# Kernel tuning notes

Measured on AMD Instinct MI355X. Metric: run time of the kernel, lower is better.

## Reference

```python
import jax, jax.numpy as jnp
import numpy as np

N = 131072       # total nodes (B graphs x P nodes)
P = 4096         # nodes per graph
B = 32           # graphs in batch
E = 2097152      # edges (avg degree 16)
IN_DIM = 64
HID = 128
OUT = 16
EPS = 1e-5
SLOPE = 0.01


def _degrees(idx):
    # structural degree, clamped to min 1 (as DGL GraphConv does)
    d = jax.ops.segment_sum(jnp.ones((E,), jnp.float32), idx, num_segments=N)
    return jnp.maximum(d, 1.0)


def _graph_conv(x, W, src, dst, ew):
    # DGL GraphConv, norm='both', bias=False, with scalar edge weights:
    # h = D_out^{-1/2} x ; m_v = sum_{(u->v)} w_e h_u ; out = (D_in^{-1/2} m) W
    h = x * jax.lax.rsqrt(_degrees(src))[:, None]
    m = jax.ops.segment_sum(ew[:, None] * h[src], dst, num_segments=N)  # [N, F]
    return (m * jax.lax.rsqrt(_degrees(dst))[:, None]) @ W


def _graph_norm(x, gamma, beta, alpha):
    # GraphNorm (Cai et al. / PyG, batch=None): stats over all nodes per feature
    mu = jnp.mean(x, axis=0)
    c = x - alpha * mu
    var = jnp.mean(c * c, axis=0)
    return c * jax.lax.rsqrt(var + EPS) * gamma + beta


def _mean_nodes(h, gid):
    # per-graph mean readout; every graph has exactly P nodes
    return jax.ops.segment_sum(h, gid, num_segments=B) / P


def setup_inputs() -> dict:
    key = jax.random.key(0)
    ks = jax.random.split(key, 8)
    src = jax.random.randint(ks[0], (E,), 0, N, dtype=jnp.int32)
    # keep edges within each 4096-node graph block (batched DGL graph)
    dst = (src // P) * P + jax.random.randint(ks[1], (E,), 0, P, dtype=jnp.int32)
    features = jax.random.normal(ks[2], (N, IN_DIM), jnp.float32)
    edge_weights = jax.random.uniform(ks[3], (E,), jnp.float32)
    # kaiming/xavier-scale init approximations
    W1 = jax.random.normal(ks[4], (IN_DIM, HID), jnp.float32) * np.sqrt(2.0 / IN_DIM)
    W2 = jax.random.normal(ks[5], (HID, HID), jnp.float32) * np.sqrt(2.0 / HID)
    Wc = jax.random.normal(ks[6], (OUT, 2 * HID), jnp.float32) * np.sqrt(1.0 / (2 * HID))
    ones = jnp.ones((HID,), jnp.float32)
    zeros = jnp.zeros((HID,), jnp.float32)
    return {
        'features': features, 'edge_weights': edge_weights, 'src': src, 'dst': dst,
        'W1': W1, 'W2': W2, 'Wc': Wc,
        'gamma1': ones, 'beta1': zeros, 'alpha1': ones,
        'gamma2': ones, 'beta2': zeros, 'alpha2': ones,
    }


def reference(features, edge_weights, src, dst, W1, W2, Wc,
              gamma1, beta1, alpha1, gamma2, beta2, alpha2):
    gid = jnp.arange(N, dtype=jnp.int32) // P  # node -> graph id
    h1 = _graph_conv(features, W1, src, dst, edge_weights)
    h1 = jax.nn.leaky_relu(_graph_norm(h1, gamma1, beta1, alpha1), SLOPE)
    r1 = _mean_nodes(h1, gid)                  # [B, HID]
    h2 = _graph_conv(h1, W2, src, dst, edge_weights)
    h2 = jax.nn.leaky_relu(_graph_norm(h2, gamma2, beta2, alpha2), SLOPE)
    r2 = _mean_nodes(h2, gid)                  # [B, HID]
    readouts = jnp.concatenate([r1, r2], axis=1)  # [B, 2*HID]
    return readouts @ Wc.T                     # [B, OUT]
```

## Files before the change

### kernel.cpp

```cpp
#include <hip/hip_runtime.h>
#include <hip/hip_fp16.h>

constexpr int NN   = 131072;
constexpr int PP   = 4096;
constexpr int BG   = 32;
constexpr int EE   = 2097152;
constexpr int IND  = 64;
constexpr int HH   = 128;
constexpr int CAP  = 81920;
constexpr float EPSV   = 1e-5f;
constexpr float SLOPEV = 0.01f;

typedef short bf16x8 __attribute__((ext_vector_type(8)));
typedef float f32x4  __attribute__((ext_vector_type(4)));
typedef float f32x2  __attribute__((ext_vector_type(2)));

__device__ __forceinline__ unsigned f2bf(float f) {
    unsigned u = __float_as_uint(f);
    return (u + 0x7FFFu + ((u >> 16) & 1u)) >> 16;
}
__device__ __forceinline__ unsigned pack2bf(float lo, float hi) {
    return f2bf(lo) | (f2bf(hi) << 16);
}
__device__ __forceinline__ float bflo(unsigned p) { return __uint_as_float(p << 16); }
__device__ __forceinline__ float bfhi(unsigned p) { return __uint_as_float(p & 0xFFFF0000u); }
__device__ __forceinline__ float w16(unsigned r) {
    return __half2float(__ushort_as_half((unsigned short)(r >> 16)));
}

template <int K>
__device__ __forceinline__ void packw_body(const float* __restrict__ W,
                                           unsigned short* __restrict__ pw, int t) {
    if (t >= K * 16) return;
    int lane = t & 63, nt = (t >> 6) & 7, kt = t >> 9;
    int kbase = kt * 32 + ((lane >> 4) & 3) * 8;
    int col   = nt * 16 + (lane & 15);
    for (int j = 0; j < 8; j++)
        pw[t * 8 + j] = (unsigned short)f2bf(W[(kbase + j) * HH + col]);
}

__global__ __launch_bounds__(256) void k_prep(const float* __restrict__ features,
                                              unsigned* __restrict__ f8x,
                                              const float* __restrict__ W1,
                                              unsigned short* __restrict__ pw1,
                                              const float* __restrict__ W2,
                                              unsigned short* __restrict__ pw2,
                                              int* __restrict__ gcur,
                                              float* __restrict__ racc,
                                              unsigned* __restrict__ csr2) {
    int b = blockIdx.x, t = threadIdx.x;
    if (b < 8192) {
        int i = b * 256 + t;
        float4 v = ((const float4*)features)[i];
        int w0 = __builtin_amdgcn_cvt_pk_fp8_f32(v.x, v.y, 0, false);
        int w1 = __builtin_amdgcn_cvt_pk_fp8_f32(v.z, v.w, w0, true);
        f8x[i] = (unsigned)w1;
        return;
    }
    if (b == 8192) {
        if (t < BG) gcur[t * 16] = t * CAP;
        for (int i = t; i < 2 * BG * HH; i += 256) racc[i] = 0.f;
        return;
    }
    if (b < 8197) { packw_body<64>(W1, pw1, (b - 8193) * 256 + t); return; }
    if (b < 8205) { packw_body<128>(W2, pw2, (b - 8197) * 256 + t); return; }
    ((uint4*)csr2)[(b - 8205) * 256 + t] = make_uint4(0, 0, 0, 0);
}

__global__ __launch_bounds__(256) void k_part(const int* __restrict__ src,
                                              const int* __restrict__ dst,
                                              const float* __restrict__ ew,
                                              int* __restrict__ gcur,
                                              uint2* __restrict__ recs) {
    __shared__ int cnt[32];
    __shared__ int start[32];
    __shared__ int gbase[32];
    __shared__ uint2 stage[4096];
    int t = threadIdx.x;
    int ebase = blockIdx.x * 4096;
    if (t < 32) cnt[t] = 0;
    __syncthreads();
    int es[16]; int ed[16]; float ev[16];
#pragma unroll
    for (int k = 0; k < 16; k++) {
        int e = ebase + k * 256 + t;
        es[k] = src[e]; ed[k] = dst[e]; ev[k] = ew[e];
        atomicAdd(&cnt[es[k] >> 12], 1);
    }
    __syncthreads();
    if (t == 0) {
        int run = 0;
        for (int g = 0; g < 32; g++) { start[g] = run; run += cnt[g]; }
    }
    __syncthreads();
    if (t < 32) {
        gbase[t] = atomicAdd(&gcur[t * 16], cnt[t]);
        cnt[t] = start[t];
    }
    __syncthreads();
#pragma unroll
    for (int k = 0; k < 16; k++) {
        int g = es[k] >> 12;
        int pos = atomicAdd(&cnt[g], 1);
        stage[pos] = make_uint2((unsigned)(es[k] & 4095) | ((unsigned)(ed[k] & 4095) << 12) |
                                ((unsigned)g << 24), __float_as_uint(ev[k]));
    }
    __syncthreads();
    for (int i = t; i < 4096; i += 256) {
        uint2 r = stage[i];
        int g = r.x >> 24;
        recs[gbase[g] + (i - start[g])] = r;
    }
}

__global__ __launch_bounds__(1024) void k_hist(const uint2* __restrict__ recs,
                                               const int* __restrict__ gcur,
                                               int* __restrict__ shist,
                                               int* __restrict__ dhist) {
    __shared__ int hs[4096];
    __shared__ int hd[4096];
    int t = threadIdx.x;
    int g = blockIdx.x >> 3, c = blockIdx.x & 7;
    int n = gcur[g * 16] - g * CAP;
    int lo = (n * c) >> 3, hi = (n * (c + 1)) >> 3;
    ((int4*)hs)[t] = make_int4(0, 0, 0, 0);
    ((int4*)hd)[t] = make_int4(0, 0, 0, 0);
    __syncthreads();
    const uint2* base = recs + (size_t)g * CAP;
    for (int i = lo + t; i < hi; i += 1024) {
        unsigned x = base[i].x;
        atomicAdd(&hs[x & 4095], 1);
        atomicAdd(&hd[(x >> 12) & 4095], 1);
    }
    __syncthreads();
    ((int4*)(shist + (size_t)blockIdx.x * 4096))[t] = ((int4*)hs)[t];
    ((int4*)(dhist + (size_t)blockIdx.x * 4096))[t] = ((int4*)hd)[t];
}

__global__ __launch_bounds__(1024) void k_offs(int* __restrict__ shist,
                                               int* __restrict__ dhist,
                                               float* __restrict__ rs_s,
                                               float* __restrict__ rsd,
                                               int* __restrict__ degd,
                                               int* __restrict__ offs) {
    __shared__ int partial[1024];
    int t = threadIdx.x, g = blockIdx.x;
    int sdeg[4] = {0, 0, 0, 0}, ddeg[4] = {0, 0, 0, 0};
#pragma unroll
    for (int c = 0; c < 8; c++) {
        int4 sv = ((const int4*)(shist + (size_t)(g * 8 + c) * 4096))[t];
        int4 dv = ((const int4*)(dhist + (size_t)(g * 8 + c) * 4096))[t];
        sdeg[0] += sv.x; sdeg[1] += sv.y; sdeg[2] += sv.z; sdeg[3] += sv.w;
        ddeg[0] += dv.x; ddeg[1] += dv.y; ddeg[2] += dv.z; ddeg[3] += dv.w;
    }
    int pdeg[4];
#pragma unroll
    for (int j = 0; j < 4; j++) {
        int idx = t * 4 + j;
        int vs = sdeg[j]; if (vs < 1) vs = 1;
        rs_s[g * PP + idx] = rsqrtf((float)vs);
        int vd = ddeg[j]; if (vd < 1) vd = 1;
        rsd[g * PP + idx]  = rsqrtf((float)vd);
        pdeg[j] = (ddeg[j] + 3) & ~3;
        degd[g * PP + idx] = pdeg[j];
    }
    partial[t] = pdeg[0] + pdeg[1] + pdeg[2] + pdeg[3];
    __syncthreads();
    for (int off = 1; off < 1024; off <<= 1) {
        int v = partial[t];
        int add = (t >= off) ? partial[t - off] : 0;
        __syncthreads();
        partial[t] = v + add;
        __syncthreads();
    }
    int run = (t == 0) ? 0 : partial[t - 1];
#pragma unroll
    for (int j = 0; j < 4; j++) {
        int idx = t * 4 + j;
        offs[g * PP + idx] = g * CAP + run;
        int nb = run;
        for (int c = 0; c < 8; c++) {
            size_t hidx = (size_t)(g * 8 + c) * 4096 + idx;
            int v = dhist[hidx];
            dhist[hidx] = nb;
            nb += v;
        }
        run += pdeg[j];
    }
}

__global__ __launch_bounds__(1024) void k_place(const uint2* __restrict__ recs,
                                                const int* __restrict__ gcur,
                                                const int* __restrict__ dhist,
                                                const float* __restrict__ rs_s,
                                                unsigned* __restrict__ csr2) {
    __shared__ int cur[4096];
    __shared__ float rss[4096];
    int t = threadIdx.x;
    int g = blockIdx.x >> 3, c = blockIdx.x & 7;
    int n = gcur[g * 16] - g * CAP;
    int lo = (n * c) >> 3, hi = (n * (c + 1)) >> 3;
    ((int4*)cur)[t] = ((const int4*)(dhist + (size_t)blockIdx.x * 4096))[t];
    ((float4*)rss)[t] = ((const float4*)(rs_s + (size_t)g * PP))[t];
    __syncthreads();
    const uint2* base = recs + (size_t)g * CAP;
    unsigned* cbase = csr2 + (size_t)g * CAP;
    for (int i = lo + t; i < hi; i += 1024) {
        uint2 r = base[i];
        int sl = r.x & 4095, dl = (r.x >> 12) & 4095;
        int pos = atomicAdd(&cur[dl], 1);
        float wf = __uint_as_float(r.y) * rss[sl];
        cbase[pos] = (unsigned)sl | ((unsigned)__half_as_ushort(__float2half(wf)) << 16);
    }
}

__global__ __launch_bounds__(256) void k_aggemm1(const unsigned* __restrict__ f8x,
                                                 const unsigned* __restrict__ csr2,
                                                 const int* __restrict__ offs,
                                                 const int* __restrict__ degd,
                                                 const float* __restrict__ rsd,
                                                 const short* __restrict__ PW,
                                                 unsigned short* __restrict__ C,
                                                 float* __restrict__ part) {
    constexpr int WP = 36;
    __shared__ unsigned lds[64 * WP];
    __shared__ float s1[HH], s2[HH];
    int t = threadIdx.x;
    if (t < HH) { s1[t] = 0.f; s2[t] = 0.f; }
    int bid = blockIdx.x;
    int xcd = bid & 7, idx = bid >> 3;
    int g = xcd * 4 + (idx >> 6);
    int node0 = g * PP + (idx & 63) * 64;
    int lane = t & 63, wv = t >> 6;
    int q = lane >> 4, ql = lane & 15;
    const unsigned* hp8 = f8x + (size_t)((unsigned)(g * PP)) * 16 + ql;
    for (int p = 0; p < 2; p++) {
        int lrA = wv * 16 + p * 8 + q * 2;
        int va = node0 + lrA, vb = va + 1;
        int oa = offs[va], ca = degd[va];
        int ob = offs[vb], cb = degd[vb];
        float A0 = 0.f, A1 = 0.f, A2 = 0.f, A3 = 0.f;
        float B0 = 0.f, B1 = 0.f, B2 = 0.f, B3 = 0.f;
        int c0 = ca < cb ? ca : cb;
        int cm = ca < cb ? cb : ca;
        int i = 0;
        for (; i < c0; i += 4) {
            uint4 ra = *(const uint4*)(csr2 + oa + i);
            uint4 rb = *(const uint4*)(csr2 + ob + i);
            unsigned qa0 = hp8[(ra.x & 4095) * 16];
            unsigned qa1 = hp8[(ra.y & 4095) * 16];
            unsigned qa2 = hp8[(ra.z & 4095) * 16];
            unsigned qa3 = hp8[(ra.w & 4095) * 16];
            unsigned qb0 = hp8[(rb.x & 4095) * 16];
            unsigned qb1 = hp8[(rb.y & 4095) * 16];
            unsigned qb2 = hp8[(rb.z & 4095) * 16];
            unsigned qb3 = hp8[(rb.w & 4095) * 16];
            {
                f32x2 lo = __builtin_amdgcn_cvt_pk_f32_fp8((int)qa0, false);
                f32x2 hi = __builtin_amdgcn_cvt_pk_f32_fp8((int)qa0, true);
                float w = w16(ra.x);
                A0 += w * lo.x; A1 += w * lo.y; A2 += w * hi.x; A3 += w * hi.y;
            }
            {
                f32x2 lo = __builtin_amdgcn_cvt_pk_f32_fp8((int)qa1, false);
                f32x2 hi = __builtin_amdgcn_cvt_pk_f32_fp8((int)qa1, true);
                float w = w16(ra.y);
                A0 += w * lo.x; A1 += w * lo.y; A2 += w * hi.x; A3 += w * hi.y;
            }
            {
                f32x2 lo = __builtin_amdgcn_cvt_pk_f32_fp8((int)qa2, false);
                f32x2 hi = __builtin_amdgcn_cvt_pk_f32_fp8((int)qa2, true);
                float w = w16(ra.z);
                A0 += w * lo.x; A1 += w * lo.y; A2 += w * hi.x; A3 += w * hi.y;
            }
            {
                f32x2 lo = __builtin_amdgcn_cvt_pk_f32_fp8((int)qa3, false);
                f32x2 hi = __builtin_amdgcn_cvt_pk_f32_fp8((int)qa3, true);
                float w = w16(ra.w);
                A0 += w * lo.x; A1 += w * lo.y; A2 += w * hi.x; A3 += w * hi.y;
            }
            {
                f32x2 lo = __builtin_amdgcn_cvt_pk_f32_fp8((int)qb0, false);
                f32x2 hi = __builtin_amdgcn_cvt_pk_f32_fp8((int)qb0, true);
                float w = w16(rb.x);
                B0 += w * lo.x; B1 += w * lo.y; B2 += w * hi.x; B3 += w * hi.y;
            }
            {
                f32x2 lo = __builtin_amdgcn_cvt_pk_f32_fp8((int)qb1, false);
                f32x2 hi = __builtin_amdgcn_cvt_pk_f32_fp8((int)qb1, true);
                float w = w16(rb.y);
                B0 += w * lo.x; B1 += w * lo.y; B2 += w * hi.x; B3 += w * hi.y;
            }
            {
                f32x2 lo = __builtin_amdgcn_cvt_pk_f32_fp8((int)qb2, false);
                f32x2 hi = __builtin_amdgcn_cvt_pk_f32_fp8((int)qb2, true);
                float w = w16(rb.z);
                B0 += w * lo.x; B1 += w * lo.y; B2 += w * hi.x; B3 += w * hi.y;
            }
            {
                f32x2 lo = __builtin_amdgcn_cvt_pk_f32_fp8((int)qb3, false);
                f32x2 hi = __builtin_amdgcn_cvt_pk_f32_fp8((int)qb3, true);
                float w = w16(rb.w);
                B0 += w * lo.x; B1 += w * lo.y; B2 += w * hi.x; B3 += w * hi.y;
            }
        }
        if (i < cm) {
            int ot = (ca > cb) ? oa : ob;
            float E0 = 0.f, E1 = 0.f, E2 = 0.f, E3 = 0.f;
            for (; i < cm; i += 4) {
                uint4 rr = *(const uint4*)(csr2 + ot + i);
                unsigned q0 = hp8[(rr.x & 4095) * 16];
                unsigned q1 = hp8[(rr.y & 4095) * 16];
                unsigned q2 = hp8[(rr.z & 4095) * 16];
                unsigned q3 = hp8[(rr.w & 4095) * 16];
                {
                    f32x2 lo = __builtin_amdgcn_cvt_pk_f32_fp8((int)q0, false);
                    f32x2 hi = __builtin_amdgcn_cvt_pk_f32_fp8((int)q0, true);
                    float w = w16(rr.x);
                    E0 += w * lo.x; E1 += w * lo.y; E2 += w * hi.x; E3 += w * hi.y;
                }
                {
                    f32x2 lo = __builtin_amdgcn_cvt_pk_f32_fp8((int)q1, false);
                    f32x2 hi = __builtin_amdgcn_cvt_pk_f32_fp8((int)q1, true);
                    float w = w16(rr.y);
                    E0 += w * lo.x; E1 += w * lo.y; E2 += w * hi.x; E3 += w * hi.y;
                }
                {
                    f32x2 lo = __builtin_amdgcn_cvt_pk_f32_fp8((int)q2, false);
                    f32x2 hi = __builtin_amdgcn_cvt_pk_f32_fp8((int)q2, true);
                    float w = w16(rr.z);
                    E0 += w * lo.x; E1 += w * lo.y; E2 += w * hi.x; E3 += w * hi.y;
                }
                {
                    f32x2 lo = __builtin_amdgcn_cvt_pk_f32_fp8((int)q3, false);
                    f32x2 hi = __builtin_amdgcn_cvt_pk_f32_fp8((int)q3, true);
                    float w = w16(rr.w);
                    E0 += w * lo.x; E1 += w * lo.y; E2 += w * hi.x; E3 += w * hi.y;
                }
            }
            if (ca > cb) { A0 += E0; A1 += E1; A2 += E2; A3 += E3; }
            else         { B0 += E0; B1 += E1; B2 += E2; B3 += E3; }
        }
        float rda = rsd[va], rdb = rsd[vb];
        *(uint2*)&lds[lrA * WP + ql * 2] =
            make_uint2(pack2bf(A0 * rda, A1 * rda), pack2bf(A2 * rda, A3 * rda));
        *(uint2*)&lds[(lrA + 1) * WP + ql * 2] =
            make_uint2(pack2bf(B0 * rdb, B1 * rdb), pack2bf(B2 * rdb, B3 * rdb));
    }
    __syncthreads();
    int m = lane & 15, quad = lane >> 4;
    bf16x8 a[2];
#pragma unroll
    for (int kt = 0; kt < 2; kt++)
        a[kt] = *(const bf16x8*)&lds[(wv * 16 + m) * WP + kt * 16 + quad * 4];
#pragma unroll
    for (int nt = 0; nt < 8; nt++) {
        f32x4 acc = {0.f, 0.f, 0.f, 0.f};
#pragma unroll
        for (int kt = 0; kt < 2; kt++) {
            bf16x8 b = *(const bf16x8*)(PW + ((size_t)(kt * 8 + nt) * 64 + lane) * 8);
            acc = __builtin_amdgcn_mfma_f32_16x16x32_bf16(a[kt], b, acc, 0, 0, 0);
        }
        int col = nt * 16 + m;
        int r0 = node0 + wv * 16 + quad * 4;
        float ps = 0.f, pq = 0.f;
#pragma unroll
        for (int r = 0; r < 4; r++) {
            C[(size_t)(r0 + r) * HH + col] = (unsigned short)f2bf(acc[r]);
            ps += acc[r]; pq += acc[r] * acc[r];
        }
        atomicAdd(&s1[col], ps);
        atomicAdd(&s2[col], pq);
    }
    __syncthreads();
    if (t < HH) {
        part[bid * 256 + t]      = s1[t];
        part[bid * 256 + HH + t] = s2[t];
    }
}

__global__ __launch_bounds__(256) void k_aggemm2(const unsigned* __restrict__ f8,
                                                 const unsigned* __restrict__ csr2,
                                                 const int* __restrict__ offs,
                                                 const int* __restrict__ degd,
                                                 const float* __restrict__ rsd,
                                                 const short* __restrict__ PW,
                                                 unsigned short* __restrict__ C,
                                                 float* __restrict__ part) {
    constexpr int WP = 68;
    __shared__ unsigned lds[64 * WP];
    __shared__ float s1[HH], s2[HH];
    int t = threadIdx.x;
    if (t < HH) { s1[t] = 0.f; s2[t] = 0.f; }
    int bid = blockIdx.x;
    int xcd = bid & 7, idx = bid >> 3;
    int g = xcd * 4 + (idx >> 6);
    int node0 = g * PP + (idx & 63) * 64;
    int lane = t & 63, wv = t >> 6;
    int half = lane >> 5, sl = lane & 31;
    const unsigned* hp8 = f8 + (size_t)((unsigned)(g * PP)) * 32 + sl;
    for (int p = 0; p < 4; p++) {
        int va = node0 + wv * 16 + p * 4 + half * 2;
        int vb = va + 1;
        int oa = offs[va], ca = degd[va];
        int ob = offs[vb], cb = degd[vb];
        float A0 = 0.f, A1 = 0.f, A2 = 0.f, A3 = 0.f;
        float B0 = 0.f, B1 = 0.f, B2 = 0.f, B3 = 0.f;
        int c0 = ca < cb ? ca : cb;
        int cm = ca < cb ? cb : ca;
        int i = 0;
        for (; i < c0; i += 4) {
            uint4 ra = *(const uint4*)(csr2 + oa + i);
            uint4 rb = *(const uint4*)(csr2 + ob + i);
            unsigned qa0 = hp8[(ra.x & 4095) * 32];
            unsigned qa1 = hp8[(ra.y & 4095) * 32];
            unsigned qa2 = hp8[(ra.z & 4095) * 32];
            unsigned qa3 = hp8[(ra.w & 4095) * 32];
            unsigned qb0 = hp8[(rb.x & 4095) * 32];
            unsigned qb1 = hp8[(rb.y & 4095) * 32];
            unsigned qb2 = hp8[(rb.z & 4095) * 32];
            unsigned qb3 = hp8[(rb.w & 4095) * 32];
            {
                f32x2 lo = __builtin_amdgcn_cvt_pk_f32_fp8((int)qa0, false);
                f32x2 hi = __builtin_amdgcn_cvt_pk_f32_fp8((int)qa0, true);
                float w = w16(ra.x);
                A0 += w * lo.x; A1 += w * lo.y; A2 += w * hi.x; A3 += w * hi.y;
            }
            {
                f32x2 lo = __builtin_amdgcn_cvt_pk_f32_fp8((int)qa1, false);
                f32x2 hi = __builtin_amdgcn_cvt_pk_f32_fp8((int)qa1, true);
                float w = w16(ra.y);
                A0 += w * lo.x; A1 += w * lo.y; A2 += w * hi.x; A3 += w * hi.y;
            }
            {
                f32x2 lo = __builtin_amdgcn_cvt_pk_f32_fp8((int)qa2, false);
                f32x2 hi = __builtin_amdgcn_cvt_pk_f32_fp8((int)qa2, true);
                float w = w16(ra.z);
                A0 += w * lo.x; A1 += w * lo.y; A2 += w * hi.x; A3 += w * hi.y;
            }
            {
                f32x2 lo = __builtin_amdgcn_cvt_pk_f32_fp8((int)qa3, false);
                f32x2 hi = __builtin_amdgcn_cvt_pk_f32_fp8((int)qa3, true);
                float w = w16(ra.w);
                A0 += w * lo.x; A1 += w * lo.y; A2 += w * hi.x; A3 += w * hi.y;
            }
            {
                f32x2 lo = __builtin_amdgcn_cvt_pk_f32_fp8((int)qb0, false);
                f32x2 hi = __builtin_amdgcn_cvt_pk_f32_fp8((int)qb0, true);
                float w = w16(rb.x);
                B0 += w * lo.x; B1 += w * lo.y; B2 += w * hi.x; B3 += w * hi.y;
            }
            {
                f32x2 lo = __builtin_amdgcn_cvt_pk_f32_fp8((int)qb1, false);
                f32x2 hi = __builtin_amdgcn_cvt_pk_f32_fp8((int)qb1, true);
                float w = w16(rb.y);
                B0 += w * lo.x; B1 += w * lo.y; B2 += w * hi.x; B3 += w * hi.y;
            }
            {
                f32x2 lo = __builtin_amdgcn_cvt_pk_f32_fp8((int)qb2, false);
                f32x2 hi = __builtin_amdgcn_cvt_pk_f32_fp8((int)qb2, true);
                float w = w16(rb.z);
                B0 += w * lo.x; B1 += w * lo.y; B2 += w * hi.x; B3 += w * hi.y;
            }
            {
                f32x2 lo = __builtin_amdgcn_cvt_pk_f32_fp8((int)qb3, false);
                f32x2 hi = __builtin_amdgcn_cvt_pk_f32_fp8((int)qb3, true);
                float w = w16(rb.w);
                B0 += w * lo.x; B1 += w * lo.y; B2 += w * hi.x; B3 += w * hi.y;
            }
        }
        if (i < cm) {
            int ot = (ca > cb) ? oa : ob;
            float E0 = 0.f, E1 = 0.f, E2 = 0.f, E3 = 0.f;
            for (; i < cm; i += 4) {
                uint4 rr = *(const uint4*)(csr2 + ot + i);
                unsigned q0 = hp8[(rr.x & 4095) * 32];
                unsigned q1 = hp8[(rr.y & 4095) * 32];
                unsigned q2 = hp8[(rr.z & 4095) * 32];
                unsigned q3 = hp8[(rr.w & 4095) * 32];
                {
                    f32x2 lo = __builtin_amdgcn_cvt_pk_f32_fp8((int)q0, false);
                    f32x2 hi = __builtin_amdgcn_cvt_pk_f32_fp8((int)q0, true);
                    float w = w16(rr.x);
                    E0 += w * lo.x; E1 += w * lo.y; E2 += w * hi.x; E3 += w * hi.y;
                }
                {
                    f32x2 lo = __builtin_amdgcn_cvt_pk_f32_fp8((int)q1, false);
                    f32x2 hi = __builtin_amdgcn_cvt_pk_f32_fp8((int)q1, true);
                    float w = w16(rr.y);
                    E0 += w * lo.x; E1 += w * lo.y; E2 += w * hi.x; E3 += w * hi.y;
                }
                {
                    f32x2 lo = __builtin_amdgcn_cvt_pk_f32_fp8((int)q2, false);
                    f32x2 hi = __builtin_amdgcn_cvt_pk_f32_fp8((int)q2, true);
                    float w = w16(rr.z);
                    E0 += w * lo.x; E1 += w * lo.y; E2 += w * hi.x; E3 += w * hi.y;
                }
                {
                    f32x2 lo = __builtin_amdgcn_cvt_pk_f32_fp8((int)q3, false);
                    f32x2 hi = __builtin_amdgcn_cvt_pk_f32_fp8((int)q3, true);
                    float w = w16(rr.w);
                    E0 += w * lo.x; E1 += w * lo.y; E2 += w * hi.x; E3 += w * hi.y;
                }
            }
            if (ca > cb) { A0 += E0; A1 += E1; A2 += E2; A3 += E3; }
            else         { B0 += E0; B1 += E1; B2 += E2; B3 += E3; }
        }
        float rda = rsd[va], rdb = rsd[vb];
        int lrA = wv * 16 + p * 4 + half * 2;
        *(uint2*)&lds[lrA * WP + sl * 2] =
            make_uint2(pack2bf(A0 * rda, A1 * rda), pack2bf(A2 * rda, A3 * rda));
        *(uint2*)&lds[(lrA + 1) * WP + sl * 2] =
            make_uint2(pack2bf(B0 * rdb, B1 * rdb), pack2bf(B2 * rdb, B3 * rdb));
    }
    __syncthreads();
    int m = lane & 15, quad = lane >> 4;
    bf16x8 a[4];
#pragma unroll
    for (int kt = 0; kt < 4; kt++)
        a[kt] = *(const bf16x8*)&lds[(wv * 16 + m) * WP + kt * 16 + quad * 4];
#pragma unroll
    for (int nt = 0; nt < 8; nt++) {
        f32x4 acc = {0.f, 0.f, 0.f, 0.f};
#pragma unroll
        for (int kt = 0; kt < 4; kt++) {
            bf16x8 b = *(const bf16x8*)(PW + ((size_t)(kt * 8 + nt) * 64 + lane) * 8);
            acc = __builtin_amdgcn_mfma_f32_16x16x32_bf16(a[kt], b, acc, 0, 0, 0);
        }
        int col = nt * 16 + m;
        int r0 = node0 + wv * 16 + quad * 4;
        float ps = 0.f, pq = 0.f;
#pragma unroll
        for (int r = 0; r < 4; r++) {
            C[(size_t)(r0 + r) * HH + col] = (unsigned short)f2bf(acc[r]);
            ps += acc[r]; pq += acc[r] * acc[r];
        }
        atomicAdd(&s1[col], ps);
        atomicAdd(&s2[col], pq);
    }
    __syncthreads();
    if (t < HH) {
        part[bid * 256 + t]      = s1[t];
        part[bid * 256 + HH + t] = s2[t];
    }
}

__global__ __launch_bounds__(256) void k_red(const float* __restrict__ part,
                                             float* __restrict__ pb) {
    int t = threadIdx.x, b = blockIdx.x;
    float s = 0.f;
    for (int r = 0; r < 32; r++) s += part[(size_t)(b * 32 + r) * 256 + t];
    pb[b * 256 + t] = s;
}

__global__ void k_coef(const float* __restrict__ pb, const float* __restrict__ gamma,
                       const float* __restrict__ beta, const float* __restrict__ alpha,
                       float* __restrict__ ab) {
    int t = threadIdx.x;
    float s = 0.f;
    for (int b = 0; b < 64; b++) s += pb[b * 256 + t];
    __shared__ float sh[256];
    sh[t] = s;
    __syncthreads();
    if (t < 128) {
        float mu = sh[t] * (1.f / NN);
        float e2 = sh[128 + t] * (1.f / NN);
        float al = alpha[t];
        float var = e2 - (2.f * al - al * al) * mu * mu;
        float a = rsqrtf(var + EPSV) * gamma[t];
        ab[t] = a;
        ab[HH + t] = beta[t] - al * mu * a;
    }
}

template <bool WRITE>
__global__ __launch_bounds__(256) void k_normro(const unsigned* __restrict__ h,
                                                const float* __restrict__ ab,
                                                float* __restrict__ racc,
                                                unsigned short* __restrict__ f8) {
    int fp = threadIdx.x & 63;
    int q  = threadIdx.x >> 6;
    int node0 = blockIdx.x * 64;
    int g = node0 / PP;
    float a0 = ab[2 * fp], a1 = ab[2 * fp + 1];
    float b0 = ab[HH + 2 * fp], b1 = ab[HH + 2 * fp + 1];
    float s0 = 0.f, s1 = 0.f;
    for (int i = q; i < 64; i += 4) {
        size_t idx = (size_t)(node0 + i) * 64 + fp;
        unsigned v = h[idx];
        float x0 = fmaf(a0, bflo(v), b0); x0 = x0 > 0.f ? x0 : SLOPEV * x0;
        float x1 = fmaf(a1, bfhi(v), b1); x1 = x1 > 0.f ? x1 : SLOPEV * x1;
        if (WRITE) f8[idx] = (unsigned short)__builtin_amdgcn_cvt_pk_fp8_f32(x0, x1, 0, false);
        s0 += x0; s1 += x1;
    }
    __shared__ float sh[512];
    sh[threadIdx.x] = s0;
    sh[256 + threadIdx.x] = s1;
    __syncthreads();
    if (q == 0) {
        float t0 = s0 + sh[64 + fp] + sh[128 + fp] + sh[192 + fp];
        float t1 = s1 + sh[256 + 64 + fp] + sh[256 + 128 + fp] + sh[256 + 192 + fp];
        atomicAdd(&racc[g * HH + 2 * fp],     t0);
        atomicAdd(&racc[g * HH + 2 * fp + 1], t1);
    }
}

__global__ void k_final(const float* __restrict__ racc1, const float* __restrict__ racc2,
                        const float* __restrict__ Wc, float* __restrict__ out) {
    int t = threadIdx.x;
    int b = t >> 4, o = t & 15;
    float acc = 0.f;
    for (int f = 0; f < HH; f++) acc += racc1[b * HH + f] * Wc[o * (2 * HH) + f];
    for (int f = 0; f < HH; f++) acc += racc2[b * HH + f] * Wc[o * (2 * HH) + HH + f];
    out[t] = acc * (1.f / PP);
}

extern "C" void kernel_launch(void* const* d_in, const int* in_sizes, int n_in,
                              void* d_out, int out_size, void* d_ws, size_t ws_size,
                              hipStream_t stream) {
    const float* features = (const float*)d_in[0];
    const float* ew       = (const float*)d_in[1];
    const int*   src      = (const int*)d_in[2];
    const int*   dst      = (const int*)d_in[3];
    const float* W1       = (const float*)d_in[4];
    const float* W2       = (const float*)d_in[5];
    const float* Wc       = (const float*)d_in[6];
    const float* gamma1   = (const float*)d_in[7];
    const float* beta1    = (const float*)d_in[8];
    const float* alpha1   = (const float*)d_in[9];
    const float* gamma2   = (const float*)d_in[10];
    const float* beta2    = (const float*)d_in[11];
    const float* alpha2   = (const float*)d_in[12];
    float* out = (float*)d_out;

    char* w = (char*)d_ws;
    int*    gcur   = (int*)(w + 0);
    float*  racc1  = (float*)(w + (16u << 10));
    float*  racc2  = (float*)(w + (32u << 10));
    float*  ab1    = (float*)(w + (48u << 10));
    float*  ab2    = (float*)(w + (52u << 10));
    unsigned short* pw1 = (unsigned short*)(w + (64u << 10));
    unsigned short* pw2 = (unsigned short*)(w + (80u << 10));
    float*  pb     = (float*)(w + (128u << 10));
    float*  rs_s   = (float*)(w + (1024u << 10));
    float*  rsd    = (float*)(w + (1536u << 10));
    int*    degd   = (int*)(w + (2048u << 10));
    int*    offs   = (int*)(w + (2560u << 10));
    float*  part   = (float*)(w + (3u << 20));
    int*    shist  = (int*)(w + (5u << 20));
    int*    dhist  = (int*)(w + (9u << 20));
    unsigned* csr2 = (unsigned*)(w + (13u << 20));
    unsigned* mbuf = (unsigned*)(w + (23u << 20));
    unsigned* hbuf = (unsigned*)(w + (55u << 20));
    uint2*    recs = (uint2*)(w + (87u << 20));
    unsigned* f8x  = (unsigned*)(w + (107u << 20));
    unsigned* f8buf= (unsigned*)(w + (123u << 20));

    k_prep<<<10765, 256, 0, stream>>>(features, f8x, W1, pw1, W2, pw2, gcur, racc1, csr2);

    k_part<<<EE / 4096, 256, 0, stream>>>(src, dst, ew, gcur, recs);
    k_hist<<<BG * 8, 1024, 0, stream>>>(recs, gcur, shist, dhist);
    k_offs<<<BG, 1024, 0, stream>>>(shist, dhist, rs_s, rsd, degd, offs);
    k_place<<<BG * 8, 1024, 0, stream>>>(recs, gcur, dhist, rs_s, csr2);

    k_aggemm1<<<NN / 64, 256, 0, stream>>>(f8x, csr2, offs, degd, rsd,
                                           (const short*)pw1, (unsigned short*)hbuf, part);
    k_red<<<64, 256, 0, stream>>>(part, pb);
    k_coef<<<1, 256, 0, stream>>>(pb, gamma1, beta1, alpha1, ab1);
    k_normro<true><<<NN / 64, 256, 0, stream>>>(hbuf, ab1, racc1, (unsigned short*)f8buf);

    k_aggemm2<<<NN / 64, 256, 0, stream>>>(f8buf, csr2, offs, degd, rsd,
                                           (const short*)pw2, (unsigned short*)mbuf, part);
    k_red<<<64, 256, 0, stream>>>(part, pb);
    k_coef<<<1, 256, 0, stream>>>(pb, gamma2, beta2, alpha2, ab2);
    k_normro<false><<<NN / 64, 256, 0, stream>>>(mbuf, ab2, racc2, nullptr);

    k_final<<<1, 512, 0, stream>>>(racc1, racc2, Wc, out);
}
```

Measured before the change: 358.4 us.

## Switch gather features from fp8 to fp16 with packed half2 accumulation

```diff
diff --git a/kernel.cpp b/kernel.cpp
--- a/kernel.cpp
+++ b/kernel.cpp
@@ -11,22 +11,11 @@
 constexpr float EPSV   = 1e-5f;
 constexpr float SLOPEV = 0.01f;
 
-typedef short bf16x8 __attribute__((ext_vector_type(8)));
+typedef _Float16 h16x8 __attribute__((ext_vector_type(8)));
 typedef float f32x4  __attribute__((ext_vector_type(4)));
-typedef float f32x2  __attribute__((ext_vector_type(2)));
-
-__device__ __forceinline__ unsigned f2bf(float f) {
-    unsigned u = __float_as_uint(f);
-    return (u + 0x7FFFu + ((u >> 16) & 1u)) >> 16;
-}
-__device__ __forceinline__ unsigned pack2bf(float lo, float hi) {
-    return f2bf(lo) | (f2bf(hi) << 16);
-}
-__device__ __forceinline__ float bflo(unsigned p) { return __uint_as_float(p << 16); }
-__device__ __forceinline__ float bfhi(unsigned p) { return __uint_as_float(p & 0xFFFF0000u); }
-__device__ __forceinline__ float w16(unsigned r) {
-    return __half2float(__ushort_as_half((unsigned short)(r >> 16)));
-}
+
+__device__ __forceinline__ __half2 bits2h(unsigned u) { __half2 h; *(unsigned*)&h = u; return h; }
+__device__ __forceinline__ unsigned h2bits(__half2 h) { return *(unsigned*)&h; }
 
 template <int K>
 __device__ __forceinline__ void packw_body(const float* __restrict__ W,
@@ -36,11 +25,11 @@
     int kbase = kt * 32 + ((lane >> 4) & 3) * 8;
     int col   = nt * 16 + (lane & 15);
     for (int j = 0; j < 8; j++)
-        pw[t * 8 + j] = (unsigned short)f2bf(W[(kbase + j) * HH + col]);
+        pw[t * 8 + j] = __half_as_ushort(__float2half_rn(W[(kbase + j) * HH + col]));
 }
 
 __global__ __launch_bounds__(256) void k_prep(const float* __restrict__ features,
-                                              unsigned* __restrict__ f8x,
+                                              unsigned* __restrict__ f16x,
                                               const float* __restrict__ W1,
                                               unsigned short* __restrict__ pw1,
                                               const float* __restrict__ W2,
@@ -52,9 +41,9 @@
     if (b < 8192) {
         int i = b * 256 + t;
         float4 v = ((const float4*)features)[i];
-        int w0 = __builtin_amdgcn_cvt_pk_fp8_f32(v.x, v.y, 0, false);
-        int w1 = __builtin_amdgcn_cvt_pk_fp8_f32(v.z, v.w, w0, true);
-        f8x[i] = (unsigned)w1;
+        __half2 lo = __floats2half2_rn(v.x, v.y);
+        __half2 hi = __floats2half2_rn(v.z, v.w);
+        ((uint2*)f16x)[i] = make_uint2(h2bits(lo), h2bits(hi));
         return;
     }
     if (b == 8192) {
@@ -214,16 +203,73 @@
     }
 }
 
-__global__ __launch_bounds__(256) void k_aggemm1(const unsigned* __restrict__ f8x,
+__device__ __forceinline__ void edge_acc(unsigned rec, uint2 q, __half2& P01, __half2& P23) {
+    unsigned wb = __builtin_amdgcn_perm(rec, rec, 0x03020302u);
+    __half2 w2 = bits2h(wb);
+    P01 = __hfma2(w2, bits2h(q.x), P01);
+    P23 = __hfma2(w2, bits2h(q.y), P23);
+}
+
+template <int ROWW>
+__device__ __forceinline__ void agg_dual(const uint2* __restrict__ gb, unsigned loff,
+                                         const uint4* __restrict__ cs4,
+                                         int oa, int ca, int ob, int cb,
+                                         __half2& A01, __half2& A23,
+                                         __half2& B01, __half2& B23) {
+    A01 = __float2half2_rn(0.f); A23 = A01; B01 = A01; B23 = A01;
+    unsigned a4 = ((unsigned)oa) >> 2, b4 = ((unsigned)ob) >> 2;
+    int c0 = ca < cb ? ca : cb;
+    int cm = ca < cb ? cb : ca;
+    int nq = c0 >> 2;
+    uint4 ra = cs4[a4], rb = cs4[b4];
+    for (int k = 0; k < nq; k++) {
+        uint2 qa0 = gb[(ra.x & 4095u) * ROWW + loff];
+        uint2 qa1 = gb[(ra.y & 4095u) * ROWW + loff];
+        uint2 qa2 = gb[(ra.z & 4095u) * ROWW + loff];
+        uint2 qa3 = gb[(ra.w & 4095u) * ROWW + loff];
+        uint2 qb0 = gb[(rb.x & 4095u) * ROWW + loff];
+        uint2 qb1 = gb[(rb.y & 4095u) * ROWW + loff];
+        uint2 qb2 = gb[(rb.z & 4095u) * ROWW + loff];
+        uint2 qb3 = gb[(rb.w & 4095u) * ROWW + loff];
+        uint4 na = cs4[a4 + k + 1];
+        uint4 nb = cs4[b4 + k + 1];
+        edge_acc(ra.x, qa0, A01, A23); edge_acc(ra.y, qa1, A01, A23);
+        edge_acc(ra.z, qa2, A01, A23); edge_acc(ra.w, qa3, A01, A23);
+        edge_acc(rb.x, qb0, B01, B23); edge_acc(rb.y, qb1, B01, B23);
+        edge_acc(rb.z, qb2, B01, B23); edge_acc(rb.w, qb3, B01, B23);
+        ra = na; rb = nb;
+    }
+    if (cm > c0) {
+        bool an = ca > cb;
+        unsigned t4 = an ? a4 : b4;
+        int kq1 = cm >> 2;
+        __half2 E01 = __float2half2_rn(0.f), E23 = E01;
+        uint4 rr = cs4[t4 + nq];
+        for (int k = nq; k < kq1; k++) {
+            uint2 q0 = gb[(rr.x & 4095u) * ROWW + loff];
+            uint2 q1 = gb[(rr.y & 4095u) * ROWW + loff];
+            uint2 q2 = gb[(rr.z & 4095u) * ROWW + loff];
+            uint2 q3 = gb[(rr.w & 4095u) * ROWW + loff];
+            uint4 nr = cs4[t4 + k + 1];
+            edge_acc(rr.x, q0, E01, E23); edge_acc(rr.y, q1, E01, E23);
+            edge_acc(rr.z, q2, E01, E23); edge_acc(rr.w, q3, E01, E23);
+            rr = nr;
+        }
+        if (an) { A01 = __hadd2(A01, E01); A23 = __hadd2(A23, E23); }
+        else    { B01 = __hadd2(B01, E01); B23 = __hadd2(B23, E23); }
+    }
+}
+
+__global__ __launch_bounds__(256) void k_aggemm1(const unsigned* __restrict__ fx,
                                                  const unsigned* __restrict__ csr2,
                                                  const int* __restrict__ offs,
                                                  const int* __restrict__ degd,
                                                  const float* __restrict__ rsd,
-                                                 const short* __restrict__ PW,
+                                                 const unsigned short* __restrict__ PW,
                                                  unsigned short* __restrict__ C,
                                                  float* __restrict__ part) {
     constexpr int WP = 36;
-    __shared__ unsigned lds[64 * WP];
+    __shared__ __align__(16) unsigned lds[64 * WP];
     __shared__ float s1[HH], s2[HH];
     int t = threadIdx.x;
     if (t < HH) { s1[t] = 0.f; s2[t] = 0.f; }
@@ -233,140 +279,42 @@
     int node0 = g * PP + (idx & 63) * 64;
     int lane = t & 63, wv = t >> 6;
     int q = lane >> 4, ql = lane & 15;
-    const unsigned* hp8 = f8x + (size_t)((unsigned)(g * PP)) * 16 + ql;
+    const uint2* gb = (const uint2*)fx + (size_t)((unsigned)(g * PP)) * 16;
+    const uint4* cs4 = (const uint4*)csr2;
     for (int p = 0; p < 2; p++) {
         int lrA = wv * 16 + p * 8 + q * 2;
-        int va = node0 + lrA, vb = va + 1;
-        int oa = offs[va], ca = degd[va];
-        int ob = offs[vb], cb = degd[vb];
-        float A0 = 0.f, A1 = 0.f, A2 = 0.f, A3 = 0.f;
-        float B0 = 0.f, B1 = 0.f, B2 = 0.f, B3 = 0.f;
-        int c0 = ca < cb ? ca : cb;
-        int cm = ca < cb ? cb : ca;
-        int i = 0;
-        for (; i < c0; i += 4) {
-            uint4 ra = *(const uint4*)(csr2 + oa + i);
-            uint4 rb = *(const uint4*)(csr2 + ob + i);
-            unsigned qa0 = hp8[(ra.x & 4095) * 16];
-            unsigned qa1 = hp8[(ra.y & 4095) * 16];
-            unsigned qa2 = hp8[(ra.z & 4095) * 16];
-            unsigned qa3 = hp8[(ra.w & 4095) * 16];
-            unsigned qb0 = hp8[(rb.x & 4095) * 16];
-            unsigned qb1 = hp8[(rb.y & 4095) * 16];
-            unsigned qb2 = hp8[(rb.z & 4095) * 16];
-            unsigned qb3 = hp8[(rb.w & 4095) * 16];
-            {
-                f32x2 lo = __builtin_amdgcn_cvt_pk_f32_fp8((int)qa0, false);
-                f32x2 hi = __builtin_amdgcn_cvt_pk_f32_fp8((int)qa0, true);
-                float w = w16(ra.x);
-                A0 += w * lo.x; A1 += w * lo.y; A2 += w * hi.x; A3 += w * hi.y;
-            }
-            {
-                f32x2 lo = __builtin_amdgcn_cvt_pk_f32_fp8((int)qa1, false);
-                f32x2 hi = __builtin_amdgcn_cvt_pk_f32_fp8((int)qa1, true);
-                float w = w16(ra.y);
-                A0 += w * lo.x; A1 += w * lo.y; A2 += w * hi.x; A3 += w * hi.y;
-            }
-            {
-                f32x2 lo = __builtin_amdgcn_cvt_pk_f32_fp8((int)qa2, false);
-                f32x2 hi = __builtin_amdgcn_cvt_pk_f32_fp8((int)qa2, true);
-                float w = w16(ra.z);
-                A0 += w * lo.x; A1 += w * lo.y; A2 += w * hi.x; A3 += w * hi.y;
-            }
-            {
-                f32x2 lo = __builtin_amdgcn_cvt_pk_f32_fp8((int)qa3, false);
-                f32x2 hi = __builtin_amdgcn_cvt_pk_f32_fp8((int)qa3, true);
-                float w = w16(ra.w);
-                A0 += w * lo.x; A1 += w * lo.y; A2 += w * hi.x; A3 += w * hi.y;
-            }
-            {
-                f32x2 lo = __builtin_amdgcn_cvt_pk_f32_fp8((int)qb0, false);
-                f32x2 hi = __builtin_amdgcn_cvt_pk_f32_fp8((int)qb0, true);
-                float w = w16(rb.x);
-                B0 += w * lo.x; B1 += w * lo.y; B2 += w * hi.x; B3 += w * hi.y;
-            }
-            {
-                f32x2 lo = __builtin_amdgcn_cvt_pk_f32_fp8((int)qb1, false);
-                f32x2 hi = __builtin_amdgcn_cvt_pk_f32_fp8((int)qb1, true);
-                float w = w16(rb.y);
-                B0 += w * lo.x; B1 += w * lo.y; B2 += w * hi.x; B3 += w * hi.y;
-            }
-            {
-                f32x2 lo = __builtin_amdgcn_cvt_pk_f32_fp8((int)qb2, false);
-                f32x2 hi = __builtin_amdgcn_cvt_pk_f32_fp8((int)qb2, true);
-                float w = w16(rb.z);
-                B0 += w * lo.x; B1 += w * lo.y; B2 += w * hi.x; B3 += w * hi.y;
-            }
-            {
-                f32x2 lo = __builtin_amdgcn_cvt_pk_f32_fp8((int)qb3, false);
-                f32x2 hi = __builtin_amdgcn_cvt_pk_f32_fp8((int)qb3, true);
-                float w = w16(rb.w);
-                B0 += w * lo.x; B1 += w * lo.y; B2 += w * hi.x; B3 += w * hi.y;
-            }
-        }
-        if (i < cm) {
-            int ot = (ca > cb) ? oa : ob;
-            float E0 = 0.f, E1 = 0.f, E2 = 0.f, E3 = 0.f;
-            for (; i < cm; i += 4) {
-                uint4 rr = *(const uint4*)(csr2 + ot + i);
-                unsigned q0 = hp8[(rr.x & 4095) * 16];
-                unsigned q1 = hp8[(rr.y & 4095) * 16];
-                unsigned q2 = hp8[(rr.z & 4095) * 16];
-                unsigned q3 = hp8[(rr.w & 4095) * 16];
-                {
-                    f32x2 lo = __builtin_amdgcn_cvt_pk_f32_fp8((int)q0, false);
-                    f32x2 hi = __builtin_amdgcn_cvt_pk_f32_fp8((int)q0, true);
-                    float w = w16(rr.x);
-                    E0 += w * lo.x; E1 += w * lo.y; E2 += w * hi.x; E3 += w * hi.y;
-                }
-                {
-                    f32x2 lo = __builtin_amdgcn_cvt_pk_f32_fp8((int)q1, false);
-                    f32x2 hi = __builtin_amdgcn_cvt_pk_f32_fp8((int)q1, true);
-                    float w = w16(rr.y);
-                    E0 += w * lo.x; E1 += w * lo.y; E2 += w * hi.x; E3 += w * hi.y;
-                }
-                {
-                    f32x2 lo = __builtin_amdgcn_cvt_pk_f32_fp8((int)q2, false);
-                    f32x2 hi = __builtin_amdgcn_cvt_pk_f32_fp8((int)q2, true);
-                    float w = w16(rr.z);
-                    E0 += w * lo.x; E1 += w * lo.y; E2 += w * hi.x; E3 += w * hi.y;
-                }
-                {
-                    f32x2 lo = __builtin_amdgcn_cvt_pk_f32_fp8((int)q3, false);
-                    f32x2 hi = __builtin_amdgcn_cvt_pk_f32_fp8((int)q3, true);
-                    float w = w16(rr.w);
-                    E0 += w * lo.x; E1 += w * lo.y; E2 += w * hi.x; E3 += w * hi.y;
-                }
-            }
-            if (ca > cb) { A0 += E0; A1 += E1; A2 += E2; A3 += E3; }
-            else         { B0 += E0; B1 += E1; B2 += E2; B3 += E3; }
-        }
-        float rda = rsd[va], rdb = rsd[vb];
-        *(uint2*)&lds[lrA * WP + ql * 2] =
-            make_uint2(pack2bf(A0 * rda, A1 * rda), pack2bf(A2 * rda, A3 * rda));
-        *(uint2*)&lds[(lrA + 1) * WP + ql * 2] =
-            make_uint2(pack2bf(B0 * rdb, B1 * rdb), pack2bf(B2 * rdb, B3 * rdb));
+        int va = node0 + lrA;
+        int2 oo = *(const int2*)(offs + va);
+        int2 dd = *(const int2*)(degd + va);
+        __half2 A01, A23, B01, B23;
+        agg_dual<16>(gb, (unsigned)ql, cs4, oo.x, dd.x, oo.y, dd.y, A01, A23, B01, B23);
+        float2 rr2 = *(const float2*)(rsd + va);
+        __half2 ha = __float2half2_rn(rr2.x), hb = __float2half2_rn(rr2.y);
+        __half2 a0 = __hmul2(A01, ha), a1 = __hmul2(A23, ha);
+        __half2 b0 = __hmul2(B01, hb), b1 = __hmul2(B23, hb);
+        *(uint2*)&lds[lrA * WP + ql * 2]       = make_uint2(h2bits(a0), h2bits(a1));
+        *(uint2*)&lds[(lrA + 1) * WP + ql * 2] = make_uint2(h2bits(b0), h2bits(b1));
     }
     __syncthreads();
     int m = lane & 15, quad = lane >> 4;
-    bf16x8 a[2];
+    h16x8 a[2];
 #pragma unroll
     for (int kt = 0; kt < 2; kt++)
-        a[kt] = *(const bf16x8*)&lds[(wv * 16 + m) * WP + kt * 16 + quad * 4];
+        a[kt] = *(const h16x8*)&lds[(wv * 16 + m) * WP + kt * 16 + quad * 4];
 #pragma unroll
     for (int nt = 0; nt < 8; nt++) {
         f32x4 acc = {0.f, 0.f, 0.f, 0.f};
 #pragma unroll
         for (int kt = 0; kt < 2; kt++) {
-            bf16x8 b = *(const bf16x8*)(PW + ((size_t)(kt * 8 + nt) * 64 + lane) * 8);
-            acc = __builtin_amdgcn_mfma_f32_16x16x32_bf16(a[kt], b, acc, 0, 0, 0);
+            h16x8 b = *(const h16x8*)(PW + ((size_t)(kt * 8 + nt) * 64 + lane) * 8);
+            acc = __builtin_amdgcn_mfma_f32_16x16x32_f16(a[kt], b, acc, 0, 0, 0);
         }
         int col = nt * 16 + m;
         int r0 = node0 + wv * 16 + quad * 4;
         float ps = 0.f, pq = 0.f;
 #pragma unroll
         for (int r = 0; r < 4; r++) {
-            C[(size_t)(r0 + r) * HH + col] = (unsigned short)f2bf(acc[r]);
+            C[(size_t)(r0 + r) * HH + col] = __half_as_ushort(__float2half_rn(acc[r]));
             ps += acc[r]; pq += acc[r] * acc[r];
         }
         atomicAdd(&s1[col], ps);
@@ -379,16 +327,16 @@
     }
 }
 
-__global__ __launch_bounds__(256) void k_aggemm2(const unsigned* __restrict__ f8,
+__global__ __launch_bounds__(256) void k_aggemm2(const unsigned* __restrict__ hsrc,
                                                  const unsigned* __restrict__ csr2,
                                                  const int* __restrict__ offs,
                                                  const int* __restrict__ degd,
                                                  const float* __restrict__ rsd,
-                                                 const short* __restrict__ PW,
+                                                 const unsigned short* __restrict__ PW,
                                                  unsigned short* __restrict__ C,
                                                  float* __restrict__ part) {
     constexpr int WP = 68;
-    __shared__ unsigned lds[64 * WP];
+    __shared__ __align__(16) unsigned lds[64 * WP];
     __shared__ float s1[HH], s2[HH];
     int t = threadIdx.x;
     if (t < HH) { s1[t] = 0.f; s2[t] = 0.f; }
@@ -398,141 +346,42 @@
     int node0 = g * PP + (idx & 63) * 64;
     int lane = t & 63, wv = t >> 6;
     int half = lane >> 5, sl = lane & 31;
-    const unsigned* hp8 = f8 + (size_t)((unsigned)(g * PP)) * 32 + sl;
+    const uint2* gb = (const uint2*)hsrc + (size_t)((unsigned)(g * PP)) * 32;
+    const uint4* cs4 = (const uint4*)csr2;
     for (int p = 0; p < 4; p++) {
-        int va = node0 + wv * 16 + p * 4 + half * 2;
-        int vb = va + 1;
-        int oa = offs[va], ca = degd[va];
-        int ob = offs[vb], cb = degd[vb];
-        float A0 = 0.f, A1 = 0.f, A2 = 0.f, A3 = 0.f;
-        float B0 = 0.f, B1 = 0.f, B2 = 0.f, B3 = 0.f;
-        int c0 = ca < cb ? ca : cb;
-        int cm = ca < cb ? cb : ca;
-        int i = 0;
-        for (; i < c0; i += 4) {
-            uint4 ra = *(const uint4*)(csr2 + oa + i);
-            uint4 rb = *(const uint4*)(csr2 + ob + i);
-            unsigned qa0 = hp8[(ra.x & 4095) * 32];
-            unsigned qa1 = hp8[(ra.y & 4095) * 32];
-            unsigned qa2 = hp8[(ra.z & 4095) * 32];
-            unsigned qa3 = hp8[(ra.w & 4095) * 32];
-            unsigned qb0 = hp8[(rb.x & 4095) * 32];
-            unsigned qb1 = hp8[(rb.y & 4095) * 32];
-            unsigned qb2 = hp8[(rb.z & 4095) * 32];
-            unsigned qb3 = hp8[(rb.w & 4095) * 32];
-            {
-                f32x2 lo = __builtin_amdgcn_cvt_pk_f32_fp8((int)qa0, false);
-                f32x2 hi = __builtin_amdgcn_cvt_pk_f32_fp8((int)qa0, true);
-                float w = w16(ra.x);
-                A0 += w * lo.x; A1 += w * lo.y; A2 += w * hi.x; A3 += w * hi.y;
-            }
-            {
-                f32x2 lo = __builtin_amdgcn_cvt_pk_f32_fp8((int)qa1, false);
-                f32x2 hi = __builtin_amdgcn_cvt_pk_f32_fp8((int)qa1, true);
-                float w = w16(ra.y);
-                A0 += w * lo.x; A1 += w * lo.y; A2 += w * hi.x; A3 += w * hi.y;
-            }
-            {
-                f32x2 lo = __builtin_amdgcn_cvt_pk_f32_fp8((int)qa2, false);
-                f32x2 hi = __builtin_amdgcn_cvt_pk_f32_fp8((int)qa2, true);
-                float w = w16(ra.z);
-                A0 += w * lo.x; A1 += w * lo.y; A2 += w * hi.x; A3 += w * hi.y;
-            }
-            {
-                f32x2 lo = __builtin_amdgcn_cvt_pk_f32_fp8((int)qa3, false);
-                f32x2 hi = __builtin_amdgcn_cvt_pk_f32_fp8((int)qa3, true);
-                float w = w16(ra.w);
-                A0 += w * lo.x; A1 += w * lo.y; A2 += w * hi.x; A3 += w * hi.y;
-            }
-            {
-                f32x2 lo = __builtin_amdgcn_cvt_pk_f32_fp8((int)qb0, false);
-                f32x2 hi = __builtin_amdgcn_cvt_pk_f32_fp8((int)qb0, true);
-                float w = w16(rb.x);
-                B0 += w * lo.x; B1 += w * lo.y; B2 += w * hi.x; B3 += w * hi.y;
-            }
-            {
-                f32x2 lo = __builtin_amdgcn_cvt_pk_f32_fp8((int)qb1, false);
-                f32x2 hi = __builtin_amdgcn_cvt_pk_f32_fp8((int)qb1, true);
-                float w = w16(rb.y);
-                B0 += w * lo.x; B1 += w * lo.y; B2 += w * hi.x; B3 += w * hi.y;
-            }
-            {
-                f32x2 lo = __builtin_amdgcn_cvt_pk_f32_fp8((int)qb2, false);
-                f32x2 hi = __builtin_amdgcn_cvt_pk_f32_fp8((int)qb2, true);
-                float w = w16(rb.z);
-                B0 += w * lo.x; B1 += w * lo.y; B2 += w * hi.x; B3 += w * hi.y;
-            }
-            {
-                f32x2 lo = __builtin_amdgcn_cvt_pk_f32_fp8((int)qb3, false);
-                f32x2 hi = __builtin_amdgcn_cvt_pk_f32_fp8((int)qb3, true);
-                float w = w16(rb.w);
-                B0 += w * lo.x; B1 += w * lo.y; B2 += w * hi.x; B3 += w * hi.y;
-            }
-        }
-        if (i < cm) {
-            int ot = (ca > cb) ? oa : ob;
-            float E0 = 0.f, E1 = 0.f, E2 = 0.f, E3 = 0.f;
-            for (; i < cm; i += 4) {
-                uint4 rr = *(const uint4*)(csr2 + ot + i);
-                unsigned q0 = hp8[(rr.x & 4095) * 32];
-                unsigned q1 = hp8[(rr.y & 4095) * 32];
-                unsigned q2 = hp8[(rr.z & 4095) * 32];
-                unsigned q3 = hp8[(rr.w & 4095) * 32];
-                {
-                    f32x2 lo = __builtin_amdgcn_cvt_pk_f32_fp8((int)q0, false);
-                    f32x2 hi = __builtin_amdgcn_cvt_pk_f32_fp8((int)q0, true);
-                    float w = w16(rr.x);
-                    E0 += w * lo.x; E1 += w * lo.y; E2 += w * hi.x; E3 += w * hi.y;
-                }
-                {
-                    f32x2 lo = __builtin_amdgcn_cvt_pk_f32_fp8((int)q1, false);
-                    f32x2 hi = __builtin_amdgcn_cvt_pk_f32_fp8((int)q1, true);
-                    float w = w16(rr.y);
-                    E0 += w * lo.x; E1 += w * lo.y; E2 += w * hi.x; E3 += w * hi.y;
-                }
-                {
-                    f32x2 lo = __builtin_amdgcn_cvt_pk_f32_fp8((int)q2, false);
-                    f32x2 hi = __builtin_amdgcn_cvt_pk_f32_fp8((int)q2, true);
-                    float w = w16(rr.z);
-                    E0 += w * lo.x; E1 += w * lo.y; E2 += w * hi.x; E3 += w * hi.y;
-                }
-                {
-                    f32x2 lo = __builtin_amdgcn_cvt_pk_f32_fp8((int)q3, false);
-                    f32x2 hi = __builtin_amdgcn_cvt_pk_f32_fp8((int)q3, true);
-                    float w = w16(rr.w);
-                    E0 += w * lo.x; E1 += w * lo.y; E2 += w * hi.x; E3 += w * hi.y;
-                }
-            }
-            if (ca > cb) { A0 += E0; A1 += E1; A2 += E2; A3 += E3; }
-            else         { B0 += E0; B1 += E1; B2 += E2; B3 += E3; }
-        }
-        float rda = rsd[va], rdb = rsd[vb];
         int lrA = wv * 16 + p * 4 + half * 2;
-        *(uint2*)&lds[lrA * WP + sl * 2] =
-            make_uint2(pack2bf(A0 * rda, A1 * rda), pack2bf(A2 * rda, A3 * rda));
-        *(uint2*)&lds[(lrA + 1) * WP + sl * 2] =
-            make_uint2(pack2bf(B0 * rdb, B1 * rdb), pack2bf(B2 * rdb, B3 * rdb));
+        int va = node0 + lrA;
+        int2 oo = *(const int2*)(offs + va);
+        int2 dd = *(const int2*)(degd + va);
+        __half2 A01, A23, B01, B23;
+        agg_dual<32>(gb, (unsigned)sl, cs4, oo.x, dd.x, oo.y, dd.y, A01, A23, B01, B23);
+        float2 rr2 = *(const float2*)(rsd + va);
+        __half2 ha = __float2half2_rn(rr2.x), hb = __float2half2_rn(rr2.y);
+        __half2 a0 = __hmul2(A01, ha), a1 = __hmul2(A23, ha);
+        __half2 b0 = __hmul2(B01, hb), b1 = __hmul2(B23, hb);
+        *(uint2*)&lds[lrA * WP + sl * 2]       = make_uint2(h2bits(a0), h2bits(a1));
+        *(uint2*)&lds[(lrA + 1) * WP + sl * 2] = make_uint2(h2bits(b0), h2bits(b1));
     }
     __syncthreads();
     int m = lane & 15, quad = lane >> 4;
-    bf16x8 a[4];
+    h16x8 a[4];
 #pragma unroll
     for (int kt = 0; kt < 4; kt++)
-        a[kt] = *(const bf16x8*)&lds[(wv * 16 + m) * WP + kt * 16 + quad * 4];
+        a[kt] = *(const h16x8*)&lds[(wv * 16 + m) * WP + kt * 16 + quad * 4];
 #pragma unroll
     for (int nt = 0; nt < 8; nt++) {
         f32x4 acc = {0.f, 0.f, 0.f, 0.f};
 #pragma unroll
         for (int kt = 0; kt < 4; kt++) {
-            bf16x8 b = *(const bf16x8*)(PW + ((size_t)(kt * 8 + nt) * 64 + lane) * 8);
-            acc = __builtin_amdgcn_mfma_f32_16x16x32_bf16(a[kt], b, acc, 0, 0, 0);
+            h16x8 b = *(const h16x8*)(PW + ((size_t)(kt * 8 + nt) * 64 + lane) * 8);
+            acc = __builtin_amdgcn_mfma_f32_16x16x32_f16(a[kt], b, acc, 0, 0, 0);
         }
         int col = nt * 16 + m;
         int r0 = node0 + wv * 16 + quad * 4;
         float ps = 0.f, pq = 0.f;
 #pragma unroll
         for (int r = 0; r < 4; r++) {
-            C[(size_t)(r0 + r) * HH + col] = (unsigned short)f2bf(acc[r]);
+            C[(size_t)(r0 + r) * HH + col] = __half_as_ushort(__float2half_rn(acc[r]));
             ps += acc[r]; pq += acc[r] * acc[r];
         }
         atomicAdd(&s1[col], ps);
@@ -577,7 +426,7 @@
 __global__ __launch_bounds__(256) void k_normro(const unsigned* __restrict__ h,
                                                 const float* __restrict__ ab,
                                                 float* __restrict__ racc,
-                                                unsigned short* __restrict__ f8) {
+                                                unsigned* __restrict__ f16o) {
     int fp = threadIdx.x & 63;
     int q  = threadIdx.x >> 6;
     int node0 = blockIdx.x * 64;
@@ -588,9 +437,13 @@
     for (int i = q; i < 64; i += 4) {
         size_t idx = (size_t)(node0 + i) * 64 + fp;
         unsigned v = h[idx];
-        float x0 = fmaf(a0, bflo(v), b0); x0 = x0 > 0.f ? x0 : SLOPEV * x0;
-        float x1 = fmaf(a1, bfhi(v), b1); x1 = x1 > 0.f ? x1 : SLOPEV * x1;
-        if (WRITE) f8[idx] = (unsigned short)__builtin_amdgcn_cvt_pk_fp8_f32(x0, x1, 0, false);
+        __half2 hv = bits2h(v);
+        float x0 = fmaf(a0, __low2float(hv),  b0); x0 = x0 > 0.f ? x0 : SLOPEV * x0;
+        float x1 = fmaf(a1, __high2float(hv), b1); x1 = x1 > 0.f ? x1 : SLOPEV * x1;
+        if (WRITE) {
+            __half2 o = __floats2half2_rn(x0, x1);
+            f16o[idx] = h2bits(o);
+        }
         s0 += x0; s1 += x1;
     }
     __shared__ float sh[512];
@@ -653,27 +506,26 @@
     unsigned* mbuf = (unsigned*)(w + (23u << 20));
     unsigned* hbuf = (unsigned*)(w + (55u << 20));
     uint2*    recs = (uint2*)(w + (87u << 20));
-    unsigned* f8x  = (unsigned*)(w + (107u << 20));
-    unsigned* f8buf= (unsigned*)(w + (123u << 20));
-
-    k_prep<<<10765, 256, 0, stream>>>(features, f8x, W1, pw1, W2, pw2, gcur, racc1, csr2);
+    unsigned* f16x = (unsigned*)(w + (107u << 20));
+
+    k_prep<<<10765, 256, 0, stream>>>(features, f16x, W1, pw1, W2, pw2, gcur, racc1, csr2);
 
     k_part<<<EE / 4096, 256, 0, stream>>>(src, dst, ew, gcur, recs);
     k_hist<<<BG * 8, 1024, 0, stream>>>(recs, gcur, shist, dhist);
     k_offs<<<BG, 1024, 0, stream>>>(shist, dhist, rs_s, rsd, degd, offs);
     k_place<<<BG * 8, 1024, 0, stream>>>(recs, gcur, dhist, rs_s, csr2);
 
-    k_aggemm1<<<NN / 64, 256, 0, stream>>>(f8x, csr2, offs, degd, rsd,
-                                           (const short*)pw1, (unsigned short*)hbuf, part);
+    k_aggemm1<<<NN / 64, 256, 0, stream>>>(f16x, csr2, offs, degd, rsd,
+                                           pw1, (unsigned short*)hbuf, part);
     k_red<<<64, 256, 0, stream>>>(part, pb);
     k_coef<<<1, 256, 0, stream>>>(pb, gamma1, beta1, alpha1, ab1);
-    k_normro<true><<<NN / 64, 256, 0, stream>>>(hbuf, ab1, racc1, (unsigned short*)f8buf);
-
-    k_aggemm2<<<NN / 64, 256, 0, stream>>>(f8buf, csr2, offs, degd, rsd,
-                                           (const short*)pw2, (unsigned short*)mbuf, part);
+    k_normro<true><<<NN / 64, 256, 0, stream>>>(hbuf, ab1, racc1, mbuf);
+
+    k_aggemm2<<<NN / 64, 256, 0, stream>>>(mbuf, csr2, offs, degd, rsd,
+                                           pw2, (unsigned short*)hbuf, part);
     k_red<<<64, 256, 0, stream>>>(part, pb);
     k_coef<<<1, 256, 0, stream>>>(pb, gamma2, beta2, alpha2, ab2);
-    k_normro<false><<<NN / 64, 256, 0, stream>>>(mbuf, ab2, racc2, nullptr);
+    k_normro<false><<<NN / 64, 256, 0, stream>>>(hbuf, ab2, racc2, nullptr);
 
     k_final<<<1, 512, 0, stream>>>(racc1, racc2, Wc, out);
 }
```

Measured after the change: 384.1 us. +7.2%, slower.
